# Optimization experiments

Measured on AMD Instinct MI355X. Metric: run time of the kernel, lower is better.

The kernel has to match this reference:

```python
import jax, jax.numpy as jnp
import numpy as np

N = 50000      # nodes
E = 800000     # edges
F_IN = 16      # feature_size
D = 96         # d_model
G = 64         # graphs per batch


def _gcn_conv(x, W, b, src, dst, dis, num_nodes):
    # PyG GCNConv: out = D^{-1/2}(A+I)D^{-1/2} X W + b (self-loops already in src/dst)
    h = x @ W                                   # [N, out]
    norm = (dis[src] * dis[dst])[:, None]       # [E+N, 1]
    msg = h[src] * norm                         # gather + scale
    agg = jax.ops.segment_sum(msg, dst, num_segments=num_nodes)
    return agg + b


def _forward(x, W_init, b_init, W1, b1, W2, b2, W3, b3, W4, b4,
             Wo1, bo1, Wo2, bo2, edge_index, batch_index):
    act = jax.nn.leaky_relu  # default negative_slope=0.01, matches nn.LeakyReLU()
    n = x.shape[0]
    # add self-loops once; degree includes self-loop (PyG gcn_norm default)
    loop = jnp.arange(n, dtype=edge_index.dtype)
    src = jnp.concatenate([edge_index[0], loop])
    dst = jnp.concatenate([edge_index[1], loop])
    deg = jax.ops.segment_sum(jnp.ones_like(src, dtype=x.dtype), dst, num_segments=n)
    dis = jax.lax.rsqrt(deg)  # deg >= 1 due to self-loops

    h = act(_gcn_conv(x, W_init, b_init, src, dst, dis, n))
    h = act(_gcn_conv(h, W1, b1, src, dst, dis, n))
    h = act(_gcn_conv(h, W2, b2, src, dst, dis, n))
    h = act(_gcn_conv(h, W3, b3, src, dst, dis, n))
    h = act(_gcn_conv(h, W4, b4, src, dst, dis, n))

    # global max + mean pooling per graph
    gmax = jax.ops.segment_max(h, batch_index, num_segments=G)
    gsum = jax.ops.segment_sum(h, batch_index, num_segments=G)
    cnt = jax.ops.segment_sum(jnp.ones((n,), dtype=h.dtype), batch_index, num_segments=G)
    gmean = gsum / jnp.maximum(cnt, 1.0)[:, None]
    pooled = jnp.concatenate([gmax, gmean], axis=1)  # [G, 2D]

    out = act(pooled @ Wo1 + bo1)  # dropout is identity in eval
    out = out @ Wo2 + bo2          # [G, 1]
    return out


def setup_inputs() -> dict:
    key = jax.random.key(0)
    ks = jax.random.split(key, 16)
    def glorot(k, shape):
        lim = float(np.sqrt(6.0 / (shape[0] + shape[1])))
        return jax.random.uniform(k, shape, jnp.float32, -lim, lim)
    inp = {
        'x': jax.random.normal(ks[0], (N, F_IN), jnp.float32),
        'edge_index': jax.random.randint(ks[1], (2, E), 0, N, dtype=jnp.int64),
        'batch_index': jnp.sort(jax.random.randint(ks[2], (N,), 0, G, dtype=jnp.int64)),
        'W_init': glorot(ks[3], (F_IN, D)), 'b_init': jnp.zeros((D,), jnp.float32),
        'W1': glorot(ks[4], (D, D)), 'b1': jnp.zeros((D,), jnp.float32),
        'W2': glorot(ks[5], (D, D)), 'b2': jnp.zeros((D,), jnp.float32),
        'W3': glorot(ks[6], (D, D)), 'b3': jnp.zeros((D,), jnp.float32),
        'W4': glorot(ks[7], (D, D)), 'b4': jnp.zeros((D,), jnp.float32),
        'Wo1': glorot(ks[8], (2 * D, D)), 'bo1': jnp.zeros((D,), jnp.float32),
        'Wo2': glorot(ks[9], (D, 1)), 'bo2': jnp.zeros((1,), jnp.float32),
    }
    return inp


def reference(x, edge_index, batch_index, W_init, b_init, W1, b1, W2, b2,
              W3, b3, W4, b4, Wo1, bo1, Wo2, bo2):
    return _forward(x, W_init, b_init, W1, b1, W2, b2, W3, b3, W4, b4,
                    Wo1, bo1, Wo2, bo2, edge_index, batch_index)
```

## Files before the change

### kernel.cpp

```cpp
#include <hip/hip_runtime.h>
#include <hip/hip_fp16.h>
#include <math.h>

#define LEAKY(x) ((x) > 0.f ? (x) : 0.01f * (x))
#define BK_SHIFT 9
#define NBMAX 128
#define BCAP 16384

typedef _Float16 half8 __attribute__((ext_vector_type(8)));
typedef float f32x4 __attribute__((ext_vector_type(4)));

__device__ __forceinline__ void add4(float4& acc, const float4& v) {
    acc.x += v.x; acc.y += v.y; acc.z += v.z; acc.w += v.w;
}

__global__ __launch_bounds__(256) void bin_kernel(const int* __restrict__ src,
                                                  const int* __restrict__ dst,
                                                  int* __restrict__ bfill,
                                                  uint2* __restrict__ tmp,
                                                  int E, int nb) {
    __shared__ int hist[NBMAX];
    __shared__ int scanbuf[NBMAX];
    __shared__ int lofs[NBMAX];
    __shared__ int adj[NBMAX];
    __shared__ uint2 buf[2048];
    __shared__ unsigned char bkt_of[2048];
    int base = blockIdx.x * 2048;
    int cnt = min(2048, E - base);
    int tid = threadIdx.x;
    for (int b = tid; b < NBMAX; b += 256) hist[b] = 0;
    __syncthreads();
    int es[8], ed[8];
#pragma unroll
    for (int k = 0; k < 8; ++k) {
        int l = tid + k * 256;
        if (l < cnt) {
            es[k] = src[base + l];
            ed[k] = dst[base + l];
            atomicAdd(&hist[ed[k] >> BK_SHIFT], 1);
        }
    }
    __syncthreads();
    if (tid < NBMAX) scanbuf[tid] = hist[tid];
    __syncthreads();
    for (int off = 1; off < NBMAX; off <<= 1) {
        int t = (tid < NBMAX && tid >= off) ? scanbuf[tid - off] : 0;
        __syncthreads();
        if (tid < NBMAX) scanbuf[tid] += t;
        __syncthreads();
    }
    if (tid < nb) {
        int cb = hist[tid];
        int start = scanbuf[tid] - cb;
        lofs[tid] = start;
        int g = (cb > 0) ? atomicAdd(&bfill[tid], cb) : 0;
        adj[tid] = tid * BCAP + g - start;
    }
    __syncthreads();
#pragma unroll
    for (int k = 0; k < 8; ++k) {
        int l = tid + k * 256;
        if (l < cnt) {
            int b = ed[k] >> BK_SHIFT;
            int r = atomicAdd(&lofs[b], 1);
            buf[r] = make_uint2((unsigned)es[k], (unsigned)ed[k]);
            bkt_of[r] = (unsigned char)b;
        }
    }
    __syncthreads();
    for (int j = tid; j < cnt; j += 256) {
        int b = bkt_of[j];
        tmp[adj[b] + j] = buf[j];
    }
}

__global__ __launch_bounds__(512) void place2(const uint2* __restrict__ tmp,
                                              const int* __restrict__ bfill,
                                              const float* __restrict__ X,
                                              float* __restrict__ dis,
                                              int* __restrict__ row_ptr,
                                              int* __restrict__ edge_src,
                                              float* __restrict__ Z0, int kq,
                                              int n, int E, int nb) {
    __shared__ int hist[512];
    __shared__ int sc[512];
    __shared__ int sbf[NBMAX];
    __shared__ int bb_s;
    int b = blockIdx.x;
    int tid = threadIdx.x;
    if (tid < NBMAX) sbf[tid] = (tid < nb) ? bfill[tid] : 0;
    hist[tid] = 0;
    __syncthreads();
    if (tid == 0) {
        int s = 0;
        for (int k = 0; k < b; ++k) s += sbf[k];
        bb_s = s;
    }
    __syncthreads();
    int bb = bb_s;
    int cnt = sbf[b];
    const uint2* mybkt = tmp + (size_t)b * BCAP;
    int node0 = b << BK_SHIFT;
    for (int j = tid; j < cnt; j += 512)
        atomicAdd(&hist[(int)mybkt[j].y - node0], 1);
    __syncthreads();
    int v = hist[tid];
    sc[tid] = v;
    __syncthreads();
    for (int off = 1; off < 512; off <<= 1) {
        int t = (tid >= off) ? sc[tid - off] : 0;
        __syncthreads();
        sc[tid] += t;
        __syncthreads();
    }
    int excl = sc[tid] - v;
    int i = node0 + tid;
    if (i < n) {
        row_ptr[i] = bb + excl;
        float di = rsqrtf((float)(v + 1));
        dis[i] = di;
        const float4* X4 = (const float4*)X;
        float4* Z4 = (float4*)Z0;
        for (int j = 0; j < kq; ++j) {
            float4 xv = X4[(size_t)i * kq + j];
            Z4[(size_t)i * kq + j] = make_float4(di * xv.x, di * xv.y, di * xv.z, di * xv.w);
        }
    }
    if (b == 0 && tid == 0) row_ptr[n] = E;
    __syncthreads();
    hist[tid] = bb + excl;
    __syncthreads();
    for (int j = tid; j < cnt; j += 512) {
        uint2 ev = mybkt[j];
        int pos = atomicAdd(&hist[(int)ev.y - node0], 1);
        edge_src[pos] = (int)ev.x;
    }
}

template <int LPN, int F4PL, int UNROLL>
__global__ __launch_bounds__(256) void agg_wave(const float* __restrict__ Z,
                                                const float* __restrict__ dis,
                                                const int* __restrict__ row_ptr,
                                                const int* __restrict__ edge_src,
                                                float* __restrict__ A, int n) {
    constexpr int GROUPS = 64 / LPN;
    constexpr int KQ = LPN * F4PL;
    int i = (blockIdx.x * 256 + threadIdx.x) >> 6;
    if (i >= n) return;
    int lane = threadIdx.x & 63;
    int g = lane / LPN;
    int c = lane % LPN;
    const float4* Z4 = (const float4*)Z;
    float di = dis[i];
    size_t base = (size_t)i * KQ + c * F4PL;
    float4 acc[F4PL];
    if (g == 0) {
#pragma unroll
        for (int j = 0; j < F4PL; ++j) acc[j] = Z4[base + j];
    } else {
#pragma unroll
        for (int j = 0; j < F4PL; ++j) acc[j] = make_float4(0.f, 0.f, 0.f, 0.f);
    }
    int re0 = row_ptr[i], re1 = row_ptr[i + 1];
#pragma unroll UNROLL
    for (int e = re0 + g; e < re1; e += GROUPS) {
        int s = edge_src[e];
        size_t sb = (size_t)s * KQ + c * F4PL;
#pragma unroll
        for (int j = 0; j < F4PL; ++j) {
            float4 xs = Z4[sb + j];
            add4(acc[j], xs);
        }
    }
#pragma unroll
    for (int m = LPN; m < 64; m <<= 1) {
#pragma unroll
        for (int j = 0; j < F4PL; ++j) {
            acc[j].x += __shfl_xor(acc[j].x, m);
            acc[j].y += __shfl_xor(acc[j].y, m);
            acc[j].z += __shfl_xor(acc[j].z, m);
            acc[j].w += __shfl_xor(acc[j].w, m);
        }
    }
    if (g == 0) {
#pragma unroll
        for (int j = 0; j < F4PL; ++j) {
            float4 o = make_float4(di * acc[j].x, di * acc[j].y,
                                   di * acc[j].z, di * acc[j].w);
            ((float4*)A)[base + j] = o;
        }
    }
}

__global__ __launch_bounds__(256) void agg_wave_h(const __half* __restrict__ Zh,
                                                  const float* __restrict__ dis,
                                                  const int* __restrict__ row_ptr,
                                                  const int* __restrict__ edge_src,
                                                  float* __restrict__ A, int n) {
    int i = (blockIdx.x * 256 + threadIdx.x) >> 6;
    if (i >= n) return;
    int lane = threadIdx.x & 63;
    int g = lane >> 3;
    int c = lane & 7;
    float di = dis[i];
    float acc[12];
    if (g == 0) {
        const uint2* zp = (const uint2*)(Zh + (size_t)i * 96 + c * 12);
#pragma unroll
        for (int k = 0; k < 3; ++k) {
            uint2 u = zp[k];
            float2 f0 = __half22float2(*(const __half2*)&u.x);
            float2 f1 = __half22float2(*(const __half2*)&u.y);
            acc[k * 4 + 0] = f0.x; acc[k * 4 + 1] = f0.y;
            acc[k * 4 + 2] = f1.x; acc[k * 4 + 3] = f1.y;
        }
    } else {
#pragma unroll
        for (int k = 0; k < 12; ++k) acc[k] = 0.f;
    }
    int re0 = row_ptr[i], re1 = row_ptr[i + 1];
#pragma unroll 4
    for (int e = re0 + g; e < re1; e += 8) {
        int s = edge_src[e];
        const uint2* zp = (const uint2*)(Zh + (size_t)s * 96 + c * 12);
        uint2 u0 = zp[0], u1 = zp[1], u2 = zp[2];
        float2 f;
        f = __half22float2(*(const __half2*)&u0.x); acc[0] += f.x; acc[1] += f.y;
        f = __half22float2(*(const __half2*)&u0.y); acc[2] += f.x; acc[3] += f.y;
        f = __half22float2(*(const __half2*)&u1.x); acc[4] += f.x; acc[5] += f.y;
        f = __half22float2(*(const __half2*)&u1.y); acc[6] += f.x; acc[7] += f.y;
        f = __half22float2(*(const __half2*)&u2.x); acc[8] += f.x; acc[9] += f.y;
        f = __half22float2(*(const __half2*)&u2.y); acc[10] += f.x; acc[11] += f.y;
    }
#pragma unroll
    for (int m = 8; m < 64; m <<= 1) {
#pragma unroll
        for (int k = 0; k < 12; ++k) acc[k] += __shfl_xor(acc[k], m);
    }
    if (g == 0) {
        float4* ap = (float4*)(A + (size_t)i * 96 + c * 12);
#pragma unroll
        for (int k = 0; k < 3; ++k)
            ap[k] = make_float4(di * acc[k * 4 + 0], di * acc[k * 4 + 1],
                                di * acc[k * 4 + 2], di * acc[k * 4 + 3]);
    }
}

template <bool SCALE, bool OUTH>
__global__ __launch_bounds__(256) void gemm_mfma(const float* __restrict__ A,
                                                 const float* __restrict__ W,
                                                 const float* __restrict__ b,
                                                 const float* __restrict__ dis,
                                                 void* __restrict__ Xn, int n) {
    constexpr int LDA = 104;
    __shared__ __align__(16) _Float16 Ah[64 * LDA];
    __shared__ __align__(16) _Float16 Wt[96 * LDA];
    int tid = threadIdx.x;
    int i0 = blockIdx.x * 64;
    for (int idx = tid; idx < 64 * 24; idx += 256) {
        int r = idx / 24, c4 = idx % 24;
        int gi = i0 + r;
        float4 v = (gi < n) ? ((const float4*)A)[(size_t)gi * 24 + c4]
                            : make_float4(0.f, 0.f, 0.f, 0.f);
        _Float16* p = &Ah[r * LDA + c4 * 4];
        p[0] = (_Float16)v.x; p[1] = (_Float16)v.y;
        p[2] = (_Float16)v.z; p[3] = (_Float16)v.w;
    }
    for (int idx = tid; idx < 96 * 24; idx += 256) {
        int k = idx / 24, c4 = idx % 24;
        float4 v = ((const float4*)W)[(size_t)k * 24 + c4];
        int nc = c4 * 4;
        Wt[(nc + 0) * LDA + k] = (_Float16)v.x;
        Wt[(nc + 1) * LDA + k] = (_Float16)v.y;
        Wt[(nc + 2) * LDA + k] = (_Float16)v.z;
        Wt[(nc + 3) * LDA + k] = (_Float16)v.w;
    }
    __syncthreads();
    int w = tid >> 6, lane = tid & 63;
    int q = lane >> 4, c = lane & 15;
    half8 af[3];
#pragma unroll
    for (int kc = 0; kc < 3; ++kc)
        af[kc] = *(const half8*)&Ah[(w * 16 + c) * LDA + kc * 32 + q * 8];
    float dvals[4];
#pragma unroll
    for (int r = 0; r < 4; ++r) {
        int gi = i0 + w * 16 + q * 4 + r;
        dvals[r] = (SCALE && gi < n) ? dis[gi] : 1.f;
    }
#pragma unroll
    for (int nt = 0; nt < 6; ++nt) {
        f32x4 acc = {0.f, 0.f, 0.f, 0.f};
#pragma unroll
        for (int kc = 0; kc < 3; ++kc) {
            half8 bf = *(const half8*)&Wt[(nt * 16 + c) * LDA + kc * 32 + q * 8];
            acc = __builtin_amdgcn_mfma_f32_16x16x32_f16(af[kc], bf, acc, 0, 0, 0);
        }
        int col = nt * 16 + c;
        float bias = b[col];
#pragma unroll
        for (int r = 0; r < 4; ++r) {
            int gi = i0 + w * 16 + q * 4 + r;
            if (gi < n) {
                float v = acc[r] + bias;
                v = LEAKY(v);
                if (SCALE) v *= dvals[r];
                if (OUTH)
                    ((_Float16*)Xn)[(size_t)gi * 96 + col] = (_Float16)v;
                else
                    ((float*)Xn)[(size_t)gi * 96 + col] = v;
            }
        }
    }
}

__global__ __launch_bounds__(192) void gemm_l0(const float* __restrict__ A,
                                               const float* __restrict__ W,
                                               const float* __restrict__ b,
                                               const float* __restrict__ dis,
                                               __half* __restrict__ Xn, int n) {
    constexpr int KQ = 4;
    __shared__ __align__(16) float4 Al[64 * KQ];
    int tid = threadIdx.x;
    int i0 = blockIdx.x * 64;
    for (int idx = tid; idx < 64 * KQ; idx += 192) {
        int gi = i0 + idx / KQ;
        Al[idx] = (gi < n) ? ((const float4*)A)[(size_t)i0 * KQ + idx]
                           : make_float4(0.f, 0.f, 0.f, 0.f);
    }
    __syncthreads();
    int fq = tid % 24;
    int g = tid / 24;
    const float4* W4 = (const float4*)W;
    float4 bb = ((const float4*)b)[fq];
    float4 acc[8];
#pragma unroll
    for (int r = 0; r < 8; ++r) acc[r] = bb;
    for (int kc = 0; kc < 16; kc += 8) {
        float4 w[8];
#pragma unroll
        for (int kk = 0; kk < 8; ++kk) w[kk] = W4[(size_t)(kc + kk) * 24 + fq];
#pragma unroll
        for (int r = 0; r < 8; ++r) {
            const float4* ar = &Al[(g * 8 + r) * KQ + (kc >> 2)];
#pragma unroll
            for (int k4 = 0; k4 < 2; ++k4) {
                float4 a = ar[k4];
                float4 w0 = w[4 * k4 + 0], w1 = w[4 * k4 + 1];
                float4 w2 = w[4 * k4 + 2], w3 = w[4 * k4 + 3];
                acc[r].x += a.x * w0.x + a.y * w1.x + a.z * w2.x + a.w * w3.x;
                acc[r].y += a.x * w0.y + a.y * w1.y + a.z * w2.y + a.w * w3.y;
                acc[r].z += a.x * w0.z + a.y * w1.z + a.z * w2.z + a.w * w3.z;
                acc[r].w += a.x * w0.w + a.y * w1.w + a.z * w2.w + a.w * w3.w;
            }
        }
    }
#pragma unroll
    for (int r = 0; r < 8; ++r) {
        int gi = i0 + g * 8 + r;
        if (gi < n) {
            float di = dis[gi];
            float4 o;
            o.x = di * LEAKY(acc[r].x); o.y = di * LEAKY(acc[r].y);
            o.z = di * LEAKY(acc[r].z); o.w = di * LEAKY(acc[r].w);
            __half2 h0 = __floats2half2_rn(o.x, o.y);
            __half2 h1 = __floats2half2_rn(o.z, o.w);
            uint2 u;
            u.x = *(unsigned*)&h0;
            u.y = *(unsigned*)&h1;
            ((uint2*)Xn)[(size_t)gi * 24 + fq] = u;
        }
    }
}

__device__ __forceinline__ int lower_bound(const int* b, int n, int v) {
    int lo = 0, hi = n;
    while (lo < hi) {
        int m = (lo + hi) >> 1;
        if (b[m] < v) lo = m + 1; else hi = m;
    }
    return lo;
}

__global__ void pool_partial(const float* __restrict__ X, const int* __restrict__ batch,
                             float* __restrict__ pmax, float* __restrict__ psum, int n) {
    int g = blockIdx.x / 8, ch = blockIdx.x % 8;
    int f = threadIdx.x;
    int s = lower_bound(batch, n, g), e = lower_bound(batch, n, g + 1);
    int len = e - s;
    int cs = s + (int)((long)len * ch / 8);
    int ce = s + (int)((long)len * (ch + 1) / 8);
    float mx = -INFINITY, sm = 0.f;
    for (int i = cs; i < ce; ++i) {
        float v = X[(size_t)i * 96 + f];
        mx = fmaxf(mx, v);
        sm += v;
    }
    pmax[(size_t)blockIdx.x * 96 + f] = mx;
    psum[(size_t)blockIdx.x * 96 + f] = sm;
}

__global__ void pool_final(const float* __restrict__ pmax, const float* __restrict__ psum,
                           const int* __restrict__ batch,
                           const float* __restrict__ Wo1, const float* __restrict__ bo1,
                           const float* __restrict__ Wo2, const float* __restrict__ bo2,
                           float* __restrict__ out, int n) {
    __shared__ float pooled[192];
    __shared__ float sh[96];
    int g = blockIdx.x, f = threadIdx.x;
    float mx = -INFINITY, sm = 0.f;
    for (int c = 0; c < 8; ++c) {
        mx = fmaxf(mx, pmax[(size_t)(g * 8 + c) * 96 + f]);
        sm += psum[(size_t)(g * 8 + c) * 96 + f];
    }
    int s = lower_bound(batch, n, g), e = lower_bound(batch, n, g + 1);
    float cnt = fmaxf((float)(e - s), 1.f);
    pooled[f] = mx;
    pooled[96 + f] = sm / cnt;
    __syncthreads();
    float acc = bo1[f];
    for (int k = 0; k < 192; ++k) acc += pooled[k] * Wo1[k * 96 + f];
    float a = LEAKY(acc);
    sh[f] = a * Wo2[f];
    __syncthreads();
    if (f == 0) {
        float sacc = 0.f;
        for (int k = 0; k < 96; ++k) sacc += sh[k];
        out[g] = sacc + bo2[0];
    }
}

extern "C" void kernel_launch(void* const* d_in, const int* in_sizes, int n_in,
                              void* d_out, int out_size, void* d_ws, size_t ws_size,
                              hipStream_t stream) {
    const float* x      = (const float*)d_in[0];
    const int*   eidx   = (const int*)d_in[1];
    const int*   batch  = (const int*)d_in[2];
    const float* W_init = (const float*)d_in[3];
    const float* b_init = (const float*)d_in[4];
    const float* W1 = (const float*)d_in[5];  const float* b1 = (const float*)d_in[6];
    const float* W2 = (const float*)d_in[7];  const float* b2 = (const float*)d_in[8];
    const float* W3 = (const float*)d_in[9];  const float* b3 = (const float*)d_in[10];
    const float* W4 = (const float*)d_in[11]; const float* b4 = (const float*)d_in[12];
    const float* Wo1 = (const float*)d_in[13]; const float* bo1 = (const float*)d_in[14];
    const float* Wo2 = (const float*)d_in[15]; const float* bo2 = (const float*)d_in[16];
    float* out = (float*)d_out;

    const int N = in_sizes[2];
    const int E = in_sizes[1] / 2;
    const int G = out_size;
    const int* src = eidx;
    const int* dst = eidx + E;

    char* ws = (char*)d_ws;
    size_t off = 0;
    auto alloc = [&](size_t bytes) {
        size_t o = off;
        off += (bytes + 255) & ~(size_t)255;
        return o;
    };
    float* dis       = (float*)(ws + alloc((size_t)N * 4));
    int*   row_ptr   = (int*)(ws + alloc((size_t)(N + 1) * 4));
    int*   bfill     = (int*)(ws + alloc(NBMAX * 4));
    int*   edge_src  = (int*)(ws + alloc((size_t)E * 4));
    float* Z0        = (float*)(ws + alloc((size_t)N * 16 * 4));
    __half* ZA       = (__half*)(ws + alloc((size_t)N * 96 * 2));
    __half* ZB       = (__half*)(ws + alloc((size_t)N * 96 * 2));
    float* H         = (float*)(ws + alloc((size_t)N * 96 * 4));
    float* Agg       = (float*)(ws + alloc((size_t)N * 96 * 4));
    float* pmax      = (float*)(ws + alloc((size_t)G * 8 * 96 * 4));
    float* psum      = (float*)(ws + alloc((size_t)G * 8 * 96 * 4));
    uint2* tmp       = (uint2*)Agg;
    (void)ws_size; (void)n_in;

    const int nbBkt  = (N + (1 << BK_SHIFT) - 1) >> BK_SHIFT;
    const int nbWave = (N + 3) / 4;
    const int nbTile = (N + 63) / 64;

    hipMemsetAsync(bfill, 0, NBMAX * 4, stream);
    bin_kernel<<<(E + 2047) / 2048, 256, 0, stream>>>(src, dst, bfill, tmp, E, nbBkt);
    place2<<<nbBkt, 512, 0, stream>>>(tmp, bfill, x, dis, row_ptr, edge_src, Z0,
                                      4, N, E, nbBkt);

    agg_wave<4, 1, 2><<<nbWave, 256, 0, stream>>>(Z0, dis, row_ptr, edge_src, Agg, N);
    gemm_l0<<<nbTile, 192, 0, stream>>>(Agg, W_init, b_init, dis, ZA, N);

    const float* Ws[4] = {W1, W2, W3, W4};
    const float* bs[4] = {b1, b2, b3, b4};
    __half* cur = ZA;
    __half* nxt = ZB;
    for (int l = 0; l < 4; ++l) {
        agg_wave_h<<<nbWave, 256, 0, stream>>>(cur, dis, row_ptr, edge_src, Agg, N);
        if (l < 3) {
            gemm_mfma<true, true><<<nbTile, 256, 0, stream>>>(Agg, Ws[l], bs[l],
                                                              dis, nxt, N);
            __half* t = cur; cur = nxt; nxt = t;
        } else {
            gemm_mfma<false, false><<<nbTile, 256, 0, stream>>>(Agg, Ws[l], bs[l],
                                                                dis, H, N);
        }
    }

    pool_partial<<<G * 8, 96, 0, stream>>>(H, batch, pmax, psum, N);
    pool_final<<<G, 96, 0, stream>>>(pmax, psum, batch, Wo1, bo1, Wo2, bo2, out, N);
}
```

Before: 380.8 us.

## Split fp16 aggregation across two waves per node and fuse pooling kernels

The half-precision aggregation kernel now gives each node two wavefronts, one per 48-feature half. Each wave has 16 edge groups of 4 lanes, where it used to have 8 groups of 8 lanes. This doubles the edge-level parallelism per wave and shortens the per-wave edge loop, at the cost of twice as many waves and more reduction shuffles. The two pooling kernels are also merged into one 384-thread kernel per graph that reduces 4 chunks in shared memory. That removes a launch and the partial buffers, but gives less pooling parallelism (64 blocks instead of 512).

```diff
diff --git a/kernel.cpp b/kernel.cpp
--- a/kernel.cpp
+++ b/kernel.cpp
@@ -192,20 +192,23 @@
     }
 }
 
-__global__ __launch_bounds__(256) void agg_wave_h(const __half* __restrict__ Zh,
-                                                  const float* __restrict__ dis,
-                                                  const int* __restrict__ row_ptr,
-                                                  const int* __restrict__ edge_src,
-                                                  float* __restrict__ A, int n) {
-    int i = (blockIdx.x * 256 + threadIdx.x) >> 6;
+__global__ __launch_bounds__(256) void agg_wave_h2(const __half* __restrict__ Zh,
+                                                   const float* __restrict__ dis,
+                                                   const int* __restrict__ row_ptr,
+                                                   const int* __restrict__ edge_src,
+                                                   float* __restrict__ A, int n) {
+    int wid = (blockIdx.x * 256 + threadIdx.x) >> 6;
+    int i = wid >> 1;
     if (i >= n) return;
+    int h = wid & 1;
     int lane = threadIdx.x & 63;
-    int g = lane >> 3;
-    int c = lane & 7;
+    int g = lane >> 2;
+    int c = lane & 3;
+    int fb = h * 48 + c * 12;
     float di = dis[i];
     float acc[12];
     if (g == 0) {
-        const uint2* zp = (const uint2*)(Zh + (size_t)i * 96 + c * 12);
+        const uint2* zp = (const uint2*)(Zh + (size_t)i * 96 + fb);
 #pragma unroll
         for (int k = 0; k < 3; ++k) {
             uint2 u = zp[k];
@@ -219,10 +222,10 @@
         for (int k = 0; k < 12; ++k) acc[k] = 0.f;
     }
     int re0 = row_ptr[i], re1 = row_ptr[i + 1];
-#pragma unroll 4
-    for (int e = re0 + g; e < re1; e += 8) {
+#pragma unroll 2
+    for (int e = re0 + g; e < re1; e += 16) {
         int s = edge_src[e];
-        const uint2* zp = (const uint2*)(Zh + (size_t)s * 96 + c * 12);
+        const uint2* zp = (const uint2*)(Zh + (size_t)s * 96 + fb);
         uint2 u0 = zp[0], u1 = zp[1], u2 = zp[2];
         float2 f;
         f = __half22float2(*(const __half2*)&u0.x); acc[0] += f.x; acc[1] += f.y;
@@ -233,12 +236,12 @@
         f = __half22float2(*(const __half2*)&u2.y); acc[10] += f.x; acc[11] += f.y;
     }
 #pragma unroll
-    for (int m = 8; m < 64; m <<= 1) {
+    for (int m = 4; m < 64; m <<= 1) {
 #pragma unroll
         for (int k = 0; k < 12; ++k) acc[k] += __shfl_xor(acc[k], m);
     }
     if (g == 0) {
-        float4* ap = (float4*)(A + (size_t)i * 96 + c * 12);
+        float4* ap = (float4*)(A + (size_t)i * 96 + fb);
 #pragma unroll
         for (int k = 0; k < 3; ++k)
             ap[k] = make_float4(di * acc[k * 4 + 0], di * acc[k * 4 + 1],
@@ -382,48 +385,49 @@
     return lo;
 }
 
-__global__ void pool_partial(const float* __restrict__ X, const int* __restrict__ batch,
-                             float* __restrict__ pmax, float* __restrict__ psum, int n) {
-    int g = blockIdx.x / 8, ch = blockIdx.x % 8;
-    int f = threadIdx.x;
+__global__ __launch_bounds__(384) void pool_fused(const float* __restrict__ H,
+                                                  const int* __restrict__ batch,
+                                                  const float* __restrict__ Wo1,
+                                                  const float* __restrict__ bo1,
+                                                  const float* __restrict__ Wo2,
+                                                  const float* __restrict__ bo2,
+                                                  float* __restrict__ out, int n) {
+    __shared__ float pm[4][96];
+    __shared__ float ps[4][96];
+    __shared__ float pooled[192];
+    __shared__ float sh[96];
+    int g = blockIdx.x;
+    int f = threadIdx.x % 96;
+    int ch = threadIdx.x / 96;
     int s = lower_bound(batch, n, g), e = lower_bound(batch, n, g + 1);
     int len = e - s;
-    int cs = s + (int)((long)len * ch / 8);
-    int ce = s + (int)((long)len * (ch + 1) / 8);
+    int cs = s + (int)((long)len * ch / 4);
+    int ce = s + (int)((long)len * (ch + 1) / 4);
     float mx = -INFINITY, sm = 0.f;
     for (int i = cs; i < ce; ++i) {
-        float v = X[(size_t)i * 96 + f];
+        float v = H[(size_t)i * 96 + f];
         mx = fmaxf(mx, v);
         sm += v;
     }
-    pmax[(size_t)blockIdx.x * 96 + f] = mx;
-    psum[(size_t)blockIdx.x * 96 + f] = sm;
-}
-
-__global__ void pool_final(const float* __restrict__ pmax, const float* __restrict__ psum,
-                           const int* __restrict__ batch,
-                           const float* __restrict__ Wo1, const float* __restrict__ bo1,
-                           const float* __restrict__ Wo2, const float* __restrict__ bo2,
-                           float* __restrict__ out, int n) {
-    __shared__ float pooled[192];
-    __shared__ float sh[96];
-    int g = blockIdx.x, f = threadIdx.x;
-    float mx = -INFINITY, sm = 0.f;
-    for (int c = 0; c < 8; ++c) {
-        mx = fmaxf(mx, pmax[(size_t)(g * 8 + c) * 96 + f]);
-        sm += psum[(size_t)(g * 8 + c) * 96 + f];
-    }
-    int s = lower_bound(batch, n, g), e = lower_bound(batch, n, g + 1);
-    float cnt = fmaxf((float)(e - s), 1.f);
-    pooled[f] = mx;
-    pooled[96 + f] = sm / cnt;
-    __syncthreads();
-    float acc = bo1[f];
-    for (int k = 0; k < 192; ++k) acc += pooled[k] * Wo1[k * 96 + f];
-    float a = LEAKY(acc);
-    sh[f] = a * Wo2[f];
-    __syncthreads();
-    if (f == 0) {
+    pm[ch][f] = mx;
+    ps[ch][f] = sm;
+    __syncthreads();
+    if (threadIdx.x < 96) {
+        float m2 = fmaxf(fmaxf(pm[0][f], pm[1][f]), fmaxf(pm[2][f], pm[3][f]));
+        float s2 = ps[0][f] + ps[1][f] + ps[2][f] + ps[3][f];
+        float cnt = fmaxf((float)len, 1.f);
+        pooled[f] = m2;
+        pooled[96 + f] = s2 / cnt;
+    }
+    __syncthreads();
+    if (threadIdx.x < 96) {
+        float acc = bo1[f];
+        for (int k = 0; k < 192; ++k) acc += pooled[k] * Wo1[k * 96 + f];
+        float a = LEAKY(acc);
+        sh[f] = a * Wo2[f];
+    }
+    __syncthreads();
+    if (threadIdx.x == 0) {
         float sacc = 0.f;
         for (int k = 0; k < 96; ++k) sacc += sh[k];
         out[g] = sacc + bo2[0];
@@ -468,14 +472,13 @@
     __half* ZB       = (__half*)(ws + alloc((size_t)N * 96 * 2));
     float* H         = (float*)(ws + alloc((size_t)N * 96 * 4));
     float* Agg       = (float*)(ws + alloc((size_t)N * 96 * 4));
-    float* pmax      = (float*)(ws + alloc((size_t)G * 8 * 96 * 4));
-    float* psum      = (float*)(ws + alloc((size_t)G * 8 * 96 * 4));
     uint2* tmp       = (uint2*)Agg;
     (void)ws_size; (void)n_in;
 
-    const int nbBkt  = (N + (1 << BK_SHIFT) - 1) >> BK_SHIFT;
-    const int nbWave = (N + 3) / 4;
-    const int nbTile = (N + 63) / 64;
+    const int nbBkt   = (N + (1 << BK_SHIFT) - 1) >> BK_SHIFT;
+    const int nbWave  = (N + 3) / 4;
+    const int nbWave2 = (2 * N + 3) / 4;
+    const int nbTile  = (N + 63) / 64;
 
     hipMemsetAsync(bfill, 0, NBMAX * 4, stream);
     bin_kernel<<<(E + 2047) / 2048, 256, 0, stream>>>(src, dst, bfill, tmp, E, nbBkt);
@@ -490,7 +493,7 @@
     __half* cur = ZA;
     __half* nxt = ZB;
     for (int l = 0; l < 4; ++l) {
-        agg_wave_h<<<nbWave, 256, 0, stream>>>(cur, dis, row_ptr, edge_src, Agg, N);
+        agg_wave_h2<<<nbWave2, 256, 0, stream>>>(cur, dis, row_ptr, edge_src, Agg, N);
         if (l < 3) {
             gemm_mfma<true, true><<<nbTile, 256, 0, stream>>>(Agg, Ws[l], bs[l],
                                                               dis, nxt, N);
@@ -501,6 +504,5 @@
         }
     }
 
-    pool_partial<<<G * 8, 96, 0, stream>>>(H, batch, pmax, psum, N);
-    pool_final<<<G, 96, 0, stream>>>(pmax, psum, batch, Wo1, bo1, Wo2, bo2, out, N);
-}
+    pool_fused<<<G, 384, 0, stream>>>(H, batch, Wo1, bo1, Wo2, bo2, out, N);
+}
```

Result: slower. 489.8 us (+28.6%).

## Fuse all GCN layers and pooling into one cooperative persistent kernel

Applied to the files above, without the earlier changes.

Replaces the chain of aggregation, GEMM and pooling launches with a single cooperative megakernel that uses grid-wide syncs between stages, with grid-stride loops over nodes and tiles. This is meant to remove per-launch overhead and inter-kernel gaps for the ~12 small kernels. In exchange, occupancy is capped by the cooperative launch, the GEMM reloads W into shared memory per tile loop only once per layer, and grid.sync costs may offset savings.

```diff
diff --git a/kernel.cpp b/kernel.cpp
--- a/kernel.cpp
+++ b/kernel.cpp
@@ -1,5 +1,6 @@
 #include <hip/hip_runtime.h>
 #include <hip/hip_fp16.h>
+#include <hip/hip_cooperative_groups.h>
 #include <math.h>
 
 #define LEAKY(x) ((x) > 0.f ? (x) : 0.01f * (x))
@@ -7,11 +8,26 @@
 #define NBMAX 128
 #define BCAP 16384
 
+namespace cg = cooperative_groups;
+
 typedef _Float16 half8 __attribute__((ext_vector_type(8)));
 typedef float f32x4 __attribute__((ext_vector_type(4)));
 
 __device__ __forceinline__ void add4(float4& acc, const float4& v) {
     acc.x += v.x; acc.y += v.y; acc.z += v.z; acc.w += v.w;
+}
+
+__device__ __forceinline__ float2 h2f(unsigned u) {
+    return __half22float2(*(const __half2*)&u);
+}
+
+__device__ __forceinline__ int lower_bound(const int* b, int n, int v) {
+    int lo = 0, hi = n;
+    while (lo < hi) {
+        int m = (lo + hi) >> 1;
+        if (b[m] < v) lo = m + 1; else hi = m;
+    }
+    return lo;
 }
 
 __global__ __launch_bounds__(256) void bin_kernel(const int* __restrict__ src,
@@ -137,135 +153,25 @@
     }
 }
 
-template <int LPN, int F4PL, int UNROLL>
-__global__ __launch_bounds__(256) void agg_wave(const float* __restrict__ Z,
-                                                const float* __restrict__ dis,
-                                                const int* __restrict__ row_ptr,
-                                                const int* __restrict__ edge_src,
-                                                float* __restrict__ A, int n) {
-    constexpr int GROUPS = 64 / LPN;
-    constexpr int KQ = LPN * F4PL;
-    int i = (blockIdx.x * 256 + threadIdx.x) >> 6;
-    if (i >= n) return;
-    int lane = threadIdx.x & 63;
-    int g = lane / LPN;
-    int c = lane % LPN;
-    const float4* Z4 = (const float4*)Z;
-    float di = dis[i];
-    size_t base = (size_t)i * KQ + c * F4PL;
-    float4 acc[F4PL];
-    if (g == 0) {
-#pragma unroll
-        for (int j = 0; j < F4PL; ++j) acc[j] = Z4[base + j];
-    } else {
-#pragma unroll
-        for (int j = 0; j < F4PL; ++j) acc[j] = make_float4(0.f, 0.f, 0.f, 0.f);
-    }
-    int re0 = row_ptr[i], re1 = row_ptr[i + 1];
-#pragma unroll UNROLL
-    for (int e = re0 + g; e < re1; e += GROUPS) {
-        int s = edge_src[e];
-        size_t sb = (size_t)s * KQ + c * F4PL;
-#pragma unroll
-        for (int j = 0; j < F4PL; ++j) {
-            float4 xs = Z4[sb + j];
-            add4(acc[j], xs);
-        }
-    }
-#pragma unroll
-    for (int m = LPN; m < 64; m <<= 1) {
-#pragma unroll
-        for (int j = 0; j < F4PL; ++j) {
-            acc[j].x += __shfl_xor(acc[j].x, m);
-            acc[j].y += __shfl_xor(acc[j].y, m);
-            acc[j].z += __shfl_xor(acc[j].z, m);
-            acc[j].w += __shfl_xor(acc[j].w, m);
-        }
-    }
-    if (g == 0) {
-#pragma unroll
-        for (int j = 0; j < F4PL; ++j) {
-            float4 o = make_float4(di * acc[j].x, di * acc[j].y,
-                                   di * acc[j].z, di * acc[j].w);
-            ((float4*)A)[base + j] = o;
-        }
-    }
-}
-
-__global__ __launch_bounds__(256) void agg_wave_h(const __half* __restrict__ Zh,
-                                                  const float* __restrict__ dis,
-                                                  const int* __restrict__ row_ptr,
-                                                  const int* __restrict__ edge_src,
-                                                  float* __restrict__ A, int n) {
-    int i = (blockIdx.x * 256 + threadIdx.x) >> 6;
-    if (i >= n) return;
-    int lane = threadIdx.x & 63;
-    int g = lane >> 3;
-    int c = lane & 7;
-    float di = dis[i];
-    float acc[12];
-    if (g == 0) {
-        const uint2* zp = (const uint2*)(Zh + (size_t)i * 96 + c * 12);
-#pragma unroll
-        for (int k = 0; k < 3; ++k) {
-            uint2 u = zp[k];
-            float2 f0 = __half22float2(*(const __half2*)&u.x);
-            float2 f1 = __half22float2(*(const __half2*)&u.y);
-            acc[k * 4 + 0] = f0.x; acc[k * 4 + 1] = f0.y;
-            acc[k * 4 + 2] = f1.x; acc[k * 4 + 3] = f1.y;
-        }
-    } else {
-#pragma unroll
-        for (int k = 0; k < 12; ++k) acc[k] = 0.f;
-    }
-    int re0 = row_ptr[i], re1 = row_ptr[i + 1];
-#pragma unroll 4
-    for (int e = re0 + g; e < re1; e += 8) {
-        int s = edge_src[e];
-        const uint2* zp = (const uint2*)(Zh + (size_t)s * 96 + c * 12);
-        uint2 u0 = zp[0], u1 = zp[1], u2 = zp[2];
-        float2 f;
-        f = __half22float2(*(const __half2*)&u0.x); acc[0] += f.x; acc[1] += f.y;
-        f = __half22float2(*(const __half2*)&u0.y); acc[2] += f.x; acc[3] += f.y;
-        f = __half22float2(*(const __half2*)&u1.x); acc[4] += f.x; acc[5] += f.y;
-        f = __half22float2(*(const __half2*)&u1.y); acc[6] += f.x; acc[7] += f.y;
-        f = __half22float2(*(const __half2*)&u2.x); acc[8] += f.x; acc[9] += f.y;
-        f = __half22float2(*(const __half2*)&u2.y); acc[10] += f.x; acc[11] += f.y;
-    }
-#pragma unroll
-    for (int m = 8; m < 64; m <<= 1) {
-#pragma unroll
-        for (int k = 0; k < 12; ++k) acc[k] += __shfl_xor(acc[k], m);
-    }
-    if (g == 0) {
-        float4* ap = (float4*)(A + (size_t)i * 96 + c * 12);
-#pragma unroll
-        for (int k = 0; k < 3; ++k)
-            ap[k] = make_float4(di * acc[k * 4 + 0], di * acc[k * 4 + 1],
-                                di * acc[k * 4 + 2], di * acc[k * 4 + 3]);
-    }
-}
-
-template <bool SCALE, bool OUTH>
-__global__ __launch_bounds__(256) void gemm_mfma(const float* __restrict__ A,
-                                                 const float* __restrict__ W,
-                                                 const float* __restrict__ b,
-                                                 const float* __restrict__ dis,
-                                                 void* __restrict__ Xn, int n) {
+struct MegaP {
+    const float* dis; const int* row_ptr; const int* edge_src; const int* batch;
+    const float* Z0; __half* ZA; __half* ZB; float* H; float* Agg;
+    float* pmax; float* psum;
+    const float* W0; const float* b0;
+    const float* W1; const float* b1;
+    const float* W2; const float* b2;
+    const float* W3; const float* b3;
+    const float* W4; const float* b4;
+    const float* Wo1; const float* bo1; const float* Wo2; const float* bo2;
+    float* out; int N; int G;
+};
+
+template <int SCALE, int OUTH>
+__device__ void gemm96(const float* A, const float* W, const float* bias,
+                       const float* dis, void* Xn, int n,
+                       _Float16* Ah, _Float16* Wt) {
     constexpr int LDA = 104;
-    __shared__ __align__(16) _Float16 Ah[64 * LDA];
-    __shared__ __align__(16) _Float16 Wt[96 * LDA];
     int tid = threadIdx.x;
-    int i0 = blockIdx.x * 64;
-    for (int idx = tid; idx < 64 * 24; idx += 256) {
-        int r = idx / 24, c4 = idx % 24;
-        int gi = i0 + r;
-        float4 v = (gi < n) ? ((const float4*)A)[(size_t)gi * 24 + c4]
-                            : make_float4(0.f, 0.f, 0.f, 0.f);
-        _Float16* p = &Ah[r * LDA + c4 * 4];
-        p[0] = (_Float16)v.x; p[1] = (_Float16)v.y;
-        p[2] = (_Float16)v.z; p[3] = (_Float16)v.w;
-    }
     for (int idx = tid; idx < 96 * 24; idx += 256) {
         int k = idx / 24, c4 = idx % 24;
         float4 v = ((const float4*)W)[(size_t)k * 24 + c4];
@@ -278,155 +184,272 @@
     __syncthreads();
     int w = tid >> 6, lane = tid & 63;
     int q = lane >> 4, c = lane & 15;
-    half8 af[3];
-#pragma unroll
-    for (int kc = 0; kc < 3; ++kc)
-        af[kc] = *(const half8*)&Ah[(w * 16 + c) * LDA + kc * 32 + q * 8];
-    float dvals[4];
-#pragma unroll
-    for (int r = 0; r < 4; ++r) {
-        int gi = i0 + w * 16 + q * 4 + r;
-        dvals[r] = (SCALE && gi < n) ? dis[gi] : 1.f;
-    }
-#pragma unroll
-    for (int nt = 0; nt < 6; ++nt) {
-        f32x4 acc = {0.f, 0.f, 0.f, 0.f};
-#pragma unroll
-        for (int kc = 0; kc < 3; ++kc) {
-            half8 bf = *(const half8*)&Wt[(nt * 16 + c) * LDA + kc * 32 + q * 8];
-            acc = __builtin_amdgcn_mfma_f32_16x16x32_f16(af[kc], bf, acc, 0, 0, 0);
-        }
-        int col = nt * 16 + c;
-        float bias = b[col];
+    int tiles = (n + 63) >> 6;
+    for (int t = blockIdx.x; t < tiles; t += gridDim.x) {
+        int i0 = t << 6;
+        for (int idx = tid; idx < 64 * 24; idx += 256) {
+            int r = idx / 24, c4 = idx % 24;
+            int gi = i0 + r;
+            float4 v = (gi < n) ? ((const float4*)A)[(size_t)gi * 24 + c4]
+                                : make_float4(0.f, 0.f, 0.f, 0.f);
+            _Float16* pp = &Ah[r * LDA + c4 * 4];
+            pp[0] = (_Float16)v.x; pp[1] = (_Float16)v.y;
+            pp[2] = (_Float16)v.z; pp[3] = (_Float16)v.w;
+        }
+        __syncthreads();
+        half8 af[3];
+#pragma unroll
+        for (int kc = 0; kc < 3; ++kc)
+            af[kc] = *(const half8*)&Ah[(w * 16 + c) * LDA + kc * 32 + q * 8];
+        float dvals[4];
 #pragma unroll
         for (int r = 0; r < 4; ++r) {
             int gi = i0 + w * 16 + q * 4 + r;
-            if (gi < n) {
-                float v = acc[r] + bias;
-                v = LEAKY(v);
-                if (SCALE) v *= dvals[r];
-                if (OUTH)
-                    ((_Float16*)Xn)[(size_t)gi * 96 + col] = (_Float16)v;
-                else
-                    ((float*)Xn)[(size_t)gi * 96 + col] = v;
-            }
-        }
-    }
-}
-
-__global__ __launch_bounds__(192) void gemm_l0(const float* __restrict__ A,
-                                               const float* __restrict__ W,
-                                               const float* __restrict__ b,
-                                               const float* __restrict__ dis,
-                                               __half* __restrict__ Xn, int n) {
-    constexpr int KQ = 4;
-    __shared__ __align__(16) float4 Al[64 * KQ];
-    int tid = threadIdx.x;
-    int i0 = blockIdx.x * 64;
-    for (int idx = tid; idx < 64 * KQ; idx += 192) {
-        int gi = i0 + idx / KQ;
-        Al[idx] = (gi < n) ? ((const float4*)A)[(size_t)i0 * KQ + idx]
-                           : make_float4(0.f, 0.f, 0.f, 0.f);
-    }
-    __syncthreads();
-    int fq = tid % 24;
-    int g = tid / 24;
-    const float4* W4 = (const float4*)W;
-    float4 bb = ((const float4*)b)[fq];
-    float4 acc[8];
-#pragma unroll
-    for (int r = 0; r < 8; ++r) acc[r] = bb;
-    for (int kc = 0; kc < 16; kc += 8) {
-        float4 w[8];
-#pragma unroll
-        for (int kk = 0; kk < 8; ++kk) w[kk] = W4[(size_t)(kc + kk) * 24 + fq];
-#pragma unroll
-        for (int r = 0; r < 8; ++r) {
-            const float4* ar = &Al[(g * 8 + r) * KQ + (kc >> 2)];
-#pragma unroll
-            for (int k4 = 0; k4 < 2; ++k4) {
-                float4 a = ar[k4];
-                float4 w0 = w[4 * k4 + 0], w1 = w[4 * k4 + 1];
-                float4 w2 = w[4 * k4 + 2], w3 = w[4 * k4 + 3];
-                acc[r].x += a.x * w0.x + a.y * w1.x + a.z * w2.x + a.w * w3.x;
-                acc[r].y += a.x * w0.y + a.y * w1.y + a.z * w2.y + a.w * w3.y;
-                acc[r].z += a.x * w0.z + a.y * w1.z + a.z * w2.z + a.w * w3.z;
-                acc[r].w += a.x * w0.w + a.y * w1.w + a.z * w2.w + a.w * w3.w;
-            }
-        }
-    }
-#pragma unroll
-    for (int r = 0; r < 8; ++r) {
-        int gi = i0 + g * 8 + r;
-        if (gi < n) {
-            float di = dis[gi];
-            float4 o;
-            o.x = di * LEAKY(acc[r].x); o.y = di * LEAKY(acc[r].y);
-            o.z = di * LEAKY(acc[r].z); o.w = di * LEAKY(acc[r].w);
-            __half2 h0 = __floats2half2_rn(o.x, o.y);
-            __half2 h1 = __floats2half2_rn(o.z, o.w);
-            uint2 u;
-            u.x = *(unsigned*)&h0;
-            u.y = *(unsigned*)&h1;
-            ((uint2*)Xn)[(size_t)gi * 24 + fq] = u;
-        }
-    }
-}
-
-__device__ __forceinline__ int lower_bound(const int* b, int n, int v) {
-    int lo = 0, hi = n;
-    while (lo < hi) {
-        int m = (lo + hi) >> 1;
-        if (b[m] < v) lo = m + 1; else hi = m;
-    }
-    return lo;
-}
-
-__global__ void pool_partial(const float* __restrict__ X, const int* __restrict__ batch,
-                             float* __restrict__ pmax, float* __restrict__ psum, int n) {
-    int g = blockIdx.x / 8, ch = blockIdx.x % 8;
-    int f = threadIdx.x;
-    int s = lower_bound(batch, n, g), e = lower_bound(batch, n, g + 1);
-    int len = e - s;
-    int cs = s + (int)((long)len * ch / 8);
-    int ce = s + (int)((long)len * (ch + 1) / 8);
-    float mx = -INFINITY, sm = 0.f;
-    for (int i = cs; i < ce; ++i) {
-        float v = X[(size_t)i * 96 + f];
-        mx = fmaxf(mx, v);
-        sm += v;
-    }
-    pmax[(size_t)blockIdx.x * 96 + f] = mx;
-    psum[(size_t)blockIdx.x * 96 + f] = sm;
-}
-
-__global__ void pool_final(const float* __restrict__ pmax, const float* __restrict__ psum,
-                           const int* __restrict__ batch,
-                           const float* __restrict__ Wo1, const float* __restrict__ bo1,
-                           const float* __restrict__ Wo2, const float* __restrict__ bo2,
-                           float* __restrict__ out, int n) {
-    __shared__ float pooled[192];
-    __shared__ float sh[96];
-    int g = blockIdx.x, f = threadIdx.x;
-    float mx = -INFINITY, sm = 0.f;
-    for (int c = 0; c < 8; ++c) {
-        mx = fmaxf(mx, pmax[(size_t)(g * 8 + c) * 96 + f]);
-        sm += psum[(size_t)(g * 8 + c) * 96 + f];
-    }
-    int s = lower_bound(batch, n, g), e = lower_bound(batch, n, g + 1);
-    float cnt = fmaxf((float)(e - s), 1.f);
-    pooled[f] = mx;
-    pooled[96 + f] = sm / cnt;
-    __syncthreads();
-    float acc = bo1[f];
-    for (int k = 0; k < 192; ++k) acc += pooled[k] * Wo1[k * 96 + f];
-    float a = LEAKY(acc);
-    sh[f] = a * Wo2[f];
-    __syncthreads();
-    if (f == 0) {
-        float sacc = 0.f;
-        for (int k = 0; k < 96; ++k) sacc += sh[k];
-        out[g] = sacc + bo2[0];
+            dvals[r] = (SCALE && gi < n) ? dis[gi] : 1.f;
+        }
+#pragma unroll
+        for (int nt = 0; nt < 6; ++nt) {
+            f32x4 acc = {0.f, 0.f, 0.f, 0.f};
+#pragma unroll
+            for (int kc = 0; kc < 3; ++kc) {
+                half8 bf = *(const half8*)&Wt[(nt * 16 + c) * LDA + kc * 32 + q * 8];
+                acc = __builtin_amdgcn_mfma_f32_16x16x32_f16(af[kc], bf, acc, 0, 0, 0);
+            }
+            int col = nt * 16 + c;
+            float bv = bias[col];
+#pragma unroll
+            for (int r = 0; r < 4; ++r) {
+                int gi = i0 + w * 16 + q * 4 + r;
+                if (gi < n) {
+                    float v = acc[r] + bv;
+                    v = LEAKY(v);
+                    if (SCALE) v *= dvals[r];
+                    if (OUTH)
+                        ((_Float16*)Xn)[(size_t)gi * 96 + col] = (_Float16)v;
+                    else
+                        ((float*)Xn)[(size_t)gi * 96 + col] = v;
+                }
+            }
+        }
+        __syncthreads();
+    }
+}
+
+__device__ void agg96(const __half* Zh, const float* dis, const int* row_ptr,
+                      const int* edge_src, float* A, int n) {
+    int wid = blockIdx.x * 4 + (threadIdx.x >> 6);
+    int lane = threadIdx.x & 63;
+    int g = lane >> 3, c = lane & 7;
+    int stride = gridDim.x * 4;
+    for (int i = wid; i < n; i += stride) {
+        float di = dis[i];
+        float acc[12];
+        if (g == 0) {
+            const uint2* zp = (const uint2*)(Zh + (size_t)i * 96 + c * 12);
+            uint2 u0 = zp[0], u1 = zp[1], u2 = zp[2];
+            float2 f;
+            f = h2f(u0.x); acc[0] = f.x;  acc[1] = f.y;
+            f = h2f(u0.y); acc[2] = f.x;  acc[3] = f.y;
+            f = h2f(u1.x); acc[4] = f.x;  acc[5] = f.y;
+            f = h2f(u1.y); acc[6] = f.x;  acc[7] = f.y;
+            f = h2f(u2.x); acc[8] = f.x;  acc[9] = f.y;
+            f = h2f(u2.y); acc[10] = f.x; acc[11] = f.y;
+        } else {
+#pragma unroll
+            for (int k = 0; k < 12; ++k) acc[k] = 0.f;
+        }
+        int re0 = row_ptr[i], re1 = row_ptr[i + 1];
+#pragma unroll 4
+        for (int e = re0 + g; e < re1; e += 8) {
+            int s = edge_src[e];
+            const uint2* zp = (const uint2*)(Zh + (size_t)s * 96 + c * 12);
+            uint2 u0 = zp[0], u1 = zp[1], u2 = zp[2];
+            float2 f;
+            f = h2f(u0.x); acc[0] += f.x;  acc[1] += f.y;
+            f = h2f(u0.y); acc[2] += f.x;  acc[3] += f.y;
+            f = h2f(u1.x); acc[4] += f.x;  acc[5] += f.y;
+            f = h2f(u1.y); acc[6] += f.x;  acc[7] += f.y;
+            f = h2f(u2.x); acc[8] += f.x;  acc[9] += f.y;
+            f = h2f(u2.y); acc[10] += f.x; acc[11] += f.y;
+        }
+#pragma unroll
+        for (int m = 8; m < 64; m <<= 1) {
+#pragma unroll
+            for (int k = 0; k < 12; ++k) acc[k] += __shfl_xor(acc[k], m);
+        }
+        if (g == 0) {
+            float4* ap = (float4*)(A + (size_t)i * 96 + c * 12);
+#pragma unroll
+            for (int k = 0; k < 3; ++k)
+                ap[k] = make_float4(di * acc[k * 4 + 0], di * acc[k * 4 + 1],
+                                    di * acc[k * 4 + 2], di * acc[k * 4 + 3]);
+        }
+    }
+}
+
+__global__ __launch_bounds__(256, 4) void gnn_mega(MegaP p) {
+    cg::grid_group grid = cg::this_grid();
+    __shared__ __align__(16) _Float16 smem[16640];
+    _Float16* Ah = smem;
+    _Float16* Wt = smem + 64 * 104;
+
+    {
+        int wid = blockIdx.x * 4 + (threadIdx.x >> 6);
+        int lane = threadIdx.x & 63;
+        int g = lane >> 2, c = lane & 3;
+        const float4* Z4 = (const float4*)p.Z0;
+        int stride = gridDim.x * 4;
+        for (int i = wid; i < p.N; i += stride) {
+            float di = p.dis[i];
+            size_t base = (size_t)i * 4 + c;
+            float4 acc = (g == 0) ? Z4[base] : make_float4(0.f, 0.f, 0.f, 0.f);
+            int re0 = p.row_ptr[i], re1 = p.row_ptr[i + 1];
+#pragma unroll 2
+            for (int e = re0 + g; e < re1; e += 16) {
+                int s = p.edge_src[e];
+                add4(acc, Z4[(size_t)s * 4 + c]);
+            }
+#pragma unroll
+            for (int m = 4; m < 64; m <<= 1) {
+                acc.x += __shfl_xor(acc.x, m);
+                acc.y += __shfl_xor(acc.y, m);
+                acc.z += __shfl_xor(acc.z, m);
+                acc.w += __shfl_xor(acc.w, m);
+            }
+            if (g == 0)
+                ((float4*)p.Agg)[base] = make_float4(di * acc.x, di * acc.y,
+                                                     di * acc.z, di * acc.w);
+        }
+    }
+    grid.sync();
+
+    {
+        float4* Al = (float4*)smem;
+        int tid = threadIdx.x;
+        int tiles = (p.N + 63) >> 6;
+        const float4* W4 = (const float4*)p.W0;
+        for (int t = blockIdx.x; t < tiles; t += gridDim.x) {
+            int i0 = t << 6;
+            {
+                int gi = i0 + (tid >> 2);
+                Al[tid] = (gi < p.N) ? ((const float4*)p.Agg)[(size_t)i0 * 4 + tid]
+                                     : make_float4(0.f, 0.f, 0.f, 0.f);
+            }
+            __syncthreads();
+            if (tid < 192) {
+                int fq = tid % 24;
+                int g2 = tid / 24;
+                float4 bb = ((const float4*)p.b0)[fq];
+                float4 acc[8];
+#pragma unroll
+                for (int r = 0; r < 8; ++r) acc[r] = bb;
+                for (int kc = 0; kc < 16; kc += 8) {
+                    float4 w[8];
+#pragma unroll
+                    for (int kk = 0; kk < 8; ++kk) w[kk] = W4[(size_t)(kc + kk) * 24 + fq];
+#pragma unroll
+                    for (int r = 0; r < 8; ++r) {
+                        const float4* ar = &Al[(g2 * 8 + r) * 4 + (kc >> 2)];
+#pragma unroll
+                        for (int k4 = 0; k4 < 2; ++k4) {
+                            float4 a = ar[k4];
+                            float4 w0 = w[4 * k4 + 0], w1 = w[4 * k4 + 1];
+                            float4 w2 = w[4 * k4 + 2], w3 = w[4 * k4 + 3];
+                            acc[r].x += a.x * w0.x + a.y * w1.x + a.z * w2.x + a.w * w3.x;
+                            acc[r].y += a.x * w0.y + a.y * w1.y + a.z * w2.y + a.w * w3.y;
+                            acc[r].z += a.x * w0.z + a.y * w1.z + a.z * w2.z + a.w * w3.z;
+                            acc[r].w += a.x * w0.w + a.y * w1.w + a.z * w2.w + a.w * w3.w;
+                        }
+                    }
+                }
+#pragma unroll
+                for (int r = 0; r < 8; ++r) {
+                    int gi = i0 + g2 * 8 + r;
+                    if (gi < p.N) {
+                        float di = p.dis[gi];
+                        float4 o;
+                        o.x = di * LEAKY(acc[r].x); o.y = di * LEAKY(acc[r].y);
+                        o.z = di * LEAKY(acc[r].z); o.w = di * LEAKY(acc[r].w);
+                        __half2 h0 = __floats2half2_rn(o.x, o.y);
+                        __half2 h1 = __floats2half2_rn(o.z, o.w);
+                        uint2 u;
+                        u.x = *(unsigned*)&h0;
+                        u.y = *(unsigned*)&h1;
+                        ((uint2*)p.ZA)[(size_t)gi * 24 + fq] = u;
+                    }
+                }
+            }
+            __syncthreads();
+        }
+    }
+    grid.sync();
+
+    const float* Ws[4] = {p.W1, p.W2, p.W3, p.W4};
+    const float* bs[4] = {p.b1, p.b2, p.b3, p.b4};
+    __half* cur = p.ZA;
+    __half* nxt = p.ZB;
+    for (int l = 0; l < 4; ++l) {
+        agg96(cur, p.dis, p.row_ptr, p.edge_src, p.Agg, p.N);
+        grid.sync();
+        if (l < 3)
+            gemm96<1, 1>(p.Agg, Ws[l], bs[l], p.dis, nxt, p.N, Ah, Wt);
+        else
+            gemm96<0, 0>(p.Agg, Ws[l], bs[l], p.dis, p.H, p.N, Ah, Wt);
+        grid.sync();
+        __half* t = cur; cur = nxt; nxt = t;
+    }
+
+    {
+        int idx = blockIdx.x * 256 + threadIdx.x;
+        int tot = p.G * 8 * 96;
+        for (int ii = idx; ii < tot; ii += gridDim.x * 256) {
+            int f = ii % 96;
+            int pr = ii / 96;
+            int g = pr / 8, ch = pr % 8;
+            int s = lower_bound(p.batch, p.N, g), e = lower_bound(p.batch, p.N, g + 1);
+            int len = e - s;
+            int cs = s + (int)((long)len * ch / 8);
+            int ce = s + (int)((long)len * (ch + 1) / 8);
+            float mx = -INFINITY, sm = 0.f;
+            for (int i = cs; i < ce; ++i) {
+                float v = p.H[(size_t)i * 96 + f];
+                mx = fmaxf(mx, v);
+                sm += v;
+            }
+            p.pmax[(size_t)pr * 96 + f] = mx;
+            p.psum[(size_t)pr * 96 + f] = sm;
+        }
+    }
+    grid.sync();
+
+    if ((int)blockIdx.x < p.G) {
+        float* pooled = (float*)smem;
+        float* sh = (float*)smem + 192;
+        int g = blockIdx.x, f = threadIdx.x;
+        if (f < 96) {
+            float mx = -INFINITY, sm = 0.f;
+            for (int c = 0; c < 8; ++c) {
+                mx = fmaxf(mx, p.pmax[(size_t)(g * 8 + c) * 96 + f]);
+                sm += p.psum[(size_t)(g * 8 + c) * 96 + f];
+            }
+            int s = lower_bound(p.batch, p.N, g), e = lower_bound(p.batch, p.N, g + 1);
+            float cnt = fmaxf((float)(e - s), 1.f);
+            pooled[f] = mx;
+            pooled[96 + f] = sm / cnt;
+        }
+        __syncthreads();
+        if (f < 96) {
+            float acc = p.bo1[f];
+            for (int k = 0; k < 192; ++k) acc += pooled[k] * p.Wo1[k * 96 + f];
+            float a = LEAKY(acc);
+            sh[f] = a * p.Wo2[f];
+        }
+        __syncthreads();
+        if (f == 0) {
+            float sacc = 0.f;
+            for (int k = 0; k < 96; ++k) sacc += sh[k];
+            p.out[g] = sacc + p.bo2[0];
+        }
     }
 }
 
@@ -474,33 +497,30 @@
     (void)ws_size; (void)n_in;
 
     const int nbBkt  = (N + (1 << BK_SHIFT) - 1) >> BK_SHIFT;
-    const int nbWave = (N + 3) / 4;
-    const int nbTile = (N + 63) / 64;
-
-    hipMemsetAsync(bfill, 0, NBMAX * 4, stream);
+
+    (void)hipMemsetAsync(bfill, 0, NBMAX * 4, stream);
     bin_kernel<<<(E + 2047) / 2048, 256, 0, stream>>>(src, dst, bfill, tmp, E, nbBkt);
     place2<<<nbBkt, 512, 0, stream>>>(tmp, bfill, x, dis, row_ptr, edge_src, Z0,
                                       4, N, E, nbBkt);
 
-    agg_wave<4, 1, 2><<<nbWave, 256, 0, stream>>>(Z0, dis, row_ptr, edge_src, Agg, N);
-    gemm_l0<<<nbTile, 192, 0, stream>>>(Agg, W_init, b_init, dis, ZA, N);
-
-    const float* Ws[4] = {W1, W2, W3, W4};
-    const float* bs[4] = {b1, b2, b3, b4};
-    __half* cur = ZA;
-    __half* nxt = ZB;
-    for (int l = 0; l < 4; ++l) {
-        agg_wave_h<<<nbWave, 256, 0, stream>>>(cur, dis, row_ptr, edge_src, Agg, N);
-        if (l < 3) {
-            gemm_mfma<true, true><<<nbTile, 256, 0, stream>>>(Agg, Ws[l], bs[l],
-                                                              dis, nxt, N);
-            __half* t = cur; cur = nxt; nxt = t;
-        } else {
-            gemm_mfma<false, false><<<nbTile, 256, 0, stream>>>(Agg, Ws[l], bs[l],
-                                                                dis, H, N);
-        }
-    }
-
-    pool_partial<<<G * 8, 96, 0, stream>>>(H, batch, pmax, psum, N);
-    pool_final<<<G, 96, 0, stream>>>(pmax, psum, batch, Wo1, bo1, Wo2, bo2, out, N);
-}
+    MegaP mp;
+    mp.dis = dis; mp.row_ptr = row_ptr; mp.edge_src = edge_src; mp.batch = batch;
+    mp.Z0 = Z0; mp.ZA = ZA; mp.ZB = ZB; mp.H = H; mp.Agg = Agg;
+    mp.pmax = pmax; mp.psum = psum;
+    mp.W0 = W_init; mp.b0 = b_init;
+    mp.W1 = W1; mp.b1 = b1; mp.W2 = W2; mp.b2 = b2;
+    mp.W3 = W3; mp.b3 = b3; mp.W4 = W4; mp.b4 = b4;
+    mp.Wo1 = Wo1; mp.bo1 = bo1; mp.Wo2 = Wo2; mp.bo2 = bo2;
+    mp.out = out; mp.N = N; mp.G = G;
+
+    int nbPerCU = 0;
+    if (hipOccupancyMaxActiveBlocksPerMultiprocessor(&nbPerCU, gnn_mega, 256, 0)
+            != hipSuccess || nbPerCU < 1)
+        nbPerCU = 2;
+    if (nbPerCU > 4) nbPerCU = 4;
+    int grid = nbPerCU * 256;
+
+    void* kargs[] = { (void*)&mp };
+    (void)hipLaunchCooperativeKernel((const void*)gnn_mega, dim3(grid), dim3(256),
+                                     kargs, 0, stream);
+}
```

Result: slower. 1.252 ms (+228.8%).
